# Optimization experiments

Measured on AMD Instinct MI355X. Metric: run time of the kernel, lower is better.

The kernel has to match this reference:

```python
import jax, jax.numpy as jnp
import numpy as np

EPS = 1e-12  # torch F.normalize clamp_min eps


def _linear_interp(t, M):
    # PyTorch F.interpolate(mode='linear', align_corners=False) along last axis.
    L = t.shape[-1]
    src = (jnp.arange(M, dtype=t.dtype) + 0.5) * (L / M) - 0.5
    src = jnp.maximum(src, 0.0)
    i0 = jnp.minimum(jnp.floor(src).astype(jnp.int32), L - 1)
    i1 = jnp.minimum(i0 + 1, L - 1)
    frac = src - i0.astype(t.dtype)
    return t[..., i0] * (1.0 - frac) + t[..., i1] * frac


def _l2norm(t):
    n = jnp.linalg.norm(t, axis=-1, keepdims=True)
    return t / jnp.maximum(n, EPS)


def setup_inputs() -> dict:
    key = jax.random.key(0)
    ks = jax.random.split(key, 6)
    b, dim, m = 4, 512, 4096
    h = w = 64
    heads = 8
    s = 0.02
    return {
        "x": jax.random.normal(ks[0], (b, dim, m), dtype=jnp.float32),
        "y": jax.random.normal(ks[1], (b, dim, h, w), dtype=jnp.float32),
        "temperature": jnp.ones((heads, 1, 1), dtype=jnp.float32),
        "w_kv": jax.random.normal(ks[2], (2 * dim, dim), dtype=jnp.float32) * s,
        "w_q": jax.random.normal(ks[3], (dim, dim), dtype=jnp.float32) * s,
        "w_dw": jax.random.normal(ks[4], (dim, dim, 3, 3), dtype=jnp.float32) * s,
        "w_out": jax.random.normal(ks[5], (dim, dim), dtype=jnp.float32) * s,
    }


def reference(x, y, temperature, w_kv, w_q, w_dw, w_out):
    b, c, m = x.shape
    heads = temperature.shape[0]
    hd = c // heads

    # kv = Conv1d(dim, 2*dim, k=1)(x); split into k, v
    kv = jnp.einsum('bcm,oc->bom', x, w_kv)
    k, v = jnp.split(kv, 2, axis=1)

    # q = dwconv3x3(Conv2d 1x1(y)) -> flatten -> linear-resize to m
    q = jnp.einsum('bchw,oc->bohw', y, w_q)
    q = jax.lax.conv_general_dilated(
        q, w_dw, window_strides=(1, 1), padding=[(1, 1), (1, 1)],
        dimension_numbers=('NCHW', 'OIHW', 'NCHW'))
    q = q.reshape(b, c, -1)
    q = _linear_interp(q, m)

    # split heads: [b, head, c', m]
    q = _l2norm(q.reshape(b, heads, hd, m))
    k = _l2norm(k.reshape(b, heads, hd, m))
    v = v.reshape(b, heads, hd, m)

    # channel-wise attention: [b, head, c', c']
    attn = jnp.einsum('bhcm,bhdm->bhcd', q, k) * temperature
    attn = jax.nn.softmax(attn, axis=-1)
    out = jnp.einsum('bhcd,bhdm->bhcm', attn, v).reshape(b, c, m)

    # project_out: Conv1d k=1
    return jnp.einsum('bcm,oc->bom', out, w_out)
```

## Files before the change

kernel.cpp:

```cpp
#include <hip/hip_runtime.h>
#include <hip/hip_bf16.h>
#include <math.h>

typedef float f32x4 __attribute__((ext_vector_type(4)));
typedef int   i32x4 __attribute__((ext_vector_type(4)));
typedef short s16x8 __attribute__((ext_vector_type(8)));

#define NB 4
#define NC 512
#define NM 4096
#define NHEADS 8

__device__ __forceinline__ float b2f(unsigned short u) {
  union { unsigned int i; float f; } x; x.i = ((unsigned)u) << 16; return x.f;
}

__global__ __launch_bounds__(256) void transpose_k(
    const float* __restrict__ x, const float* __restrict__ y,
    __hip_bfloat16* __restrict__ xT, __hip_bfloat16* __restrict__ yT)
{
  __shared__ __hip_bfloat16 tile[64][65];
  int z = blockIdx.z;
  const float* src = ((z < 4) ? x : y) + (long)(z & 3) * ((long)NC * NM);
  __hip_bfloat16* dst = (z < 4 ? xT : yT) + (long)(z & 3) * ((long)NC * NM);
  int tm = blockIdx.x * 64, tc = blockIdx.y * 64;
  int tx = threadIdx.x & 63, ty = threadIdx.x >> 6;
  #pragma unroll
  for (int p = 0; p < 16; p++) {
    int row = ty + p * 4;
    tile[row][tx] = __float2bfloat16(src[(long)(tc + row) * NM + tm + tx]);
  }
  __syncthreads();
  #pragma unroll
  for (int p = 0; p < 16; p++) {
    int row = ty + p * 4;
    dst[(long)(tm + row) * NC + tc + tx] = tile[tx][row];
  }
}

__global__ __launch_bounds__(256) void pack_wdw(
    const float* __restrict__ wdw, __hip_bfloat16* __restrict__ Wr)
{
  long idx = (long)blockIdx.x * 256 + threadIdx.x;
  if (idx < 9L * 512 * 512) {
    int r = (int)(idx >> 18);
    int rem = (int)(idx & 262143);
    int o = rem >> 9, i = rem & 511;
    Wr[idx] = __float2bfloat16(wdw[((long)o * 512 + i) * 9 + r]);
  }
}

__global__ __launch_bounds__(256) void convert_w(
    const float* __restrict__ wkv, const float* __restrict__ wq,
    __hip_bfloat16* __restrict__ wkvB, __hip_bfloat16* __restrict__ wqB)
{
  long idx = (long)blockIdx.x * 256 + threadIdx.x;
  if (idx < 524288) {
    wkvB[idx] = __float2bfloat16(wkv[idx]);
  } else if (idx < 524288 + 262144) {
    long j = idx - 524288;
    wqB[j] = __float2bfloat16(wq[j]);
  }
}

__global__ __launch_bounds__(256) void gemm_bt(
    const __hip_bfloat16* __restrict__ Aall, long sA,
    const __hip_bfloat16* __restrict__ Ball, long sB,
    __hip_bfloat16* __restrict__ Cball, float* __restrict__ Cfall, long sC,
    int M, int N, int Kd, int outF32)
{
  const __hip_bfloat16* A = Aall + (long)blockIdx.z * sA;
  const __hip_bfloat16* B = Ball + (long)blockIdx.z * sB;
  const int m0 = blockIdx.y * 128, n0 = blockIdx.x * 128;
  __shared__ __hip_bfloat16 As[128 * 40];
  __shared__ __hip_bfloat16 Bs[128 * 40];
  const int tid = threadIdx.x;
  const int wid = tid >> 6, lane = tid & 63;
  const int wm = (wid >> 1) * 64, wn = (wid & 1) * 64;
  const int quad = lane >> 4, l16 = lane & 15;
  const int srow = tid >> 2, scol = (tid & 3) * 8;
  f32x4 acc[4][4] = {};
  const __hip_bfloat16* pA0 = A + (long)(m0 + srow) * Kd + scol;
  const __hip_bfloat16* pA1 = pA0 + (long)64 * Kd;
  const __hip_bfloat16* pB0 = B + (long)(n0 + srow) * Kd + scol;
  const __hip_bfloat16* pB1 = pB0 + (long)64 * Kd;
  i32x4 va0 = *(const i32x4*)(pA0);
  i32x4 va1 = *(const i32x4*)(pA1);
  i32x4 vb0 = *(const i32x4*)(pB0);
  i32x4 vb1 = *(const i32x4*)(pB1);
  for (int k0 = 0; k0 < Kd; k0 += 32) {
    __syncthreads();
    *(i32x4*)(&As[srow * 40 + scol])        = va0;
    *(i32x4*)(&As[(srow + 64) * 40 + scol]) = va1;
    *(i32x4*)(&Bs[srow * 40 + scol])        = vb0;
    *(i32x4*)(&Bs[(srow + 64) * 40 + scol]) = vb1;
    if (k0 + 32 < Kd) {
      va0 = *(const i32x4*)(pA0 + k0 + 32);
      va1 = *(const i32x4*)(pA1 + k0 + 32);
      vb0 = *(const i32x4*)(pB0 + k0 + 32);
      vb1 = *(const i32x4*)(pB1 + k0 + 32);
    }
    __syncthreads();
    s16x8 bfr[4];
    #pragma unroll
    for (int j = 0; j < 4; j++)
      bfr[j] = *(const s16x8*)(&Bs[(wn + j * 16 + l16) * 40 + quad * 8]);
    #pragma unroll
    for (int i = 0; i < 4; i++) {
      s16x8 af = *(const s16x8*)(&As[(wm + i * 16 + l16) * 40 + quad * 8]);
      #pragma unroll
      for (int j = 0; j < 4; j++)
        acc[i][j] = __builtin_amdgcn_mfma_f32_16x16x32_bf16(af, bfr[j], acc[i][j], 0, 0, 0);
    }
  }
  if (outF32) {
    float* C = Cfall + (long)blockIdx.z * sC;
    #pragma unroll
    for (int i = 0; i < 4; i++)
      #pragma unroll
      for (int j = 0; j < 4; j++) {
        int rbase = m0 + wm + i * 16 + quad * 4;
        int col = n0 + wn + j * 16 + l16;
        #pragma unroll
        for (int r = 0; r < 4; r++)
          C[(long)(rbase + r) * N + col] = acc[i][j][r];
      }
  } else {
    __hip_bfloat16* C = Cball + (long)blockIdx.z * sC;
    #pragma unroll
    for (int i = 0; i < 4; i++)
      #pragma unroll
      for (int j = 0; j < 4; j++) {
        int rbase = m0 + wm + i * 16 + quad * 4;
        int col = n0 + wn + j * 16 + l16;
        #pragma unroll
        for (int r = 0; r < 4; r++)
          C[(long)(rbase + r) * N + col] = __float2bfloat16(acc[i][j][r]);
      }
  }
}

__global__ __launch_bounds__(256) void conv3x3(
    const __hip_bfloat16* __restrict__ Wr,
    const __hip_bfloat16* __restrict__ q1t,
    __hip_bfloat16* __restrict__ q2)
{
  const int b = blockIdx.z;
  const int n0 = blockIdx.x * 128;
  const int m0 = blockIdx.y * 128;
  __shared__ __hip_bfloat16 As[128 * 40];
  __shared__ __hip_bfloat16 Bs[256 * 40];
  const int tid = threadIdx.x;
  const int wid = tid >> 6, lane = tid & 63;
  const int wm = (wid >> 1) * 64, wn = (wid & 1) * 64;
  const int quad = lane >> 4, l16 = lane & 15;
  const int srow = tid >> 2, scol = (tid & 3) * 8;
  const int h0 = n0 >> 6;
  const __hip_bfloat16* qb = q1t + (long)b * NM * NC;
  f32x4 acc[4][4] = {};
  const s16x8 zero8 = {0, 0, 0, 0, 0, 0, 0, 0};

  for (int ic = 0; ic < 512; ic += 32) {
    __syncthreads();
    #pragma unroll
    for (int rr = 0; rr < 4; rr++) {
      int p = rr * 64 + srow;
      int hw = (h0 - 1) * 64 + p;
      i32x4 val = {};
      if (hw >= 0 && hw < NM) val = *(const i32x4*)(&qb[(long)hw * NC + ic + scol]);
      *(i32x4*)(&Bs[p * 40 + scol]) = val;
    }
    for (int r = 0; r < 9; r++) {
      int dy = r / 3 - 1, dx = r % 3 - 1;
      __syncthreads();
      *(i32x4*)(&As[srow * 40 + scol]) =
          *(const i32x4*)(&Wr[((long)r * 512 + m0 + srow) * 512 + ic + scol]);
      *(i32x4*)(&As[(srow + 64) * 40 + scol]) =
          *(const i32x4*)(&Wr[((long)r * 512 + m0 + srow + 64) * 512 + ic + scol]);
      __syncthreads();
      s16x8 bfr[4];
      #pragma unroll
      for (int j = 0; j < 4; j++) {
        int nl = wn + j * 16 + l16;
        int wq = nl & 63, hr = nl >> 6;
        int wp = wq + dx;
        bool v = ((unsigned)wp) < 64u;
        int p = v ? ((hr + 1 + dy) * 64 + wp) : 0;
        s16x8 t = *(const s16x8*)(&Bs[p * 40 + quad * 8]);
        bfr[j] = v ? t : zero8;
      }
      #pragma unroll
      for (int i = 0; i < 4; i++) {
        s16x8 af = *(const s16x8*)(&As[(wm + i * 16 + l16) * 40 + quad * 8]);
        #pragma unroll
        for (int j = 0; j < 4; j++)
          acc[i][j] = __builtin_amdgcn_mfma_f32_16x16x32_bf16(af, bfr[j], acc[i][j], 0, 0, 0);
      }
    }
  }
  __hip_bfloat16* Cb = q2 + (long)b * NC * NM;
  #pragma unroll
  for (int i = 0; i < 4; i++) {
    #pragma unroll
    for (int j = 0; j < 4; j++) {
      int rbase = m0 + wm + i * 16 + quad * 4;
      int col = n0 + wn + j * 16 + l16;
      #pragma unroll
      for (int r = 0; r < 4; r++)
        Cb[(long)(rbase + r) * NM + col] = __float2bfloat16(acc[i][j][r]);
    }
  }
}

__global__ __launch_bounds__(256) void rowsumsq(
    const __hip_bfloat16* __restrict__ X, float* __restrict__ out)
{
  long row = blockIdx.x;
  const __hip_bfloat16* p = X + row * (long)NM + threadIdx.x * 16;
  union { i32x4 v; unsigned short u[8]; } a, b;
  a.v = *(const i32x4*)(p);
  b.v = *(const i32x4*)(p + 8);
  float s = 0.f;
  #pragma unroll
  for (int t = 0; t < 8; t++) {
    float f0 = b2f(a.u[t]); s += f0 * f0;
    float f1 = b2f(b.u[t]); s += f1 * f1;
  }
  #pragma unroll
  for (int off = 32; off > 0; off >>= 1) s += __shfl_down(s, off);
  __shared__ float red[4];
  if ((threadIdx.x & 63) == 0) red[threadIdx.x >> 6] = s;
  __syncthreads();
  if (threadIdx.x == 0)
    out[row] = fmaxf(sqrtf(red[0] + red[1] + red[2] + red[3]), 1e-12f);
}

__global__ __launch_bounds__(256) void attn_g(
    const __hip_bfloat16* __restrict__ q2, const __hip_bfloat16* __restrict__ Kb,
    float* __restrict__ Gpart)
{
  const int mc = blockIdx.x, h = blockIdx.y, b = blockIdx.z;
  const __hip_bfloat16* qrow = q2 + ((long)b * NC + h * 64) * NM + mc * 512;
  const __hip_bfloat16* krow = Kb + ((long)b * NC + h * 64) * NM + mc * 512;
  __shared__ __hip_bfloat16 Qs[64 * 40];
  __shared__ __hip_bfloat16 Ks[64 * 40];
  const int tid = threadIdx.x;
  const int wid = tid >> 6, lane = tid & 63;
  const int wc = (wid >> 1) * 32, wd = (wid & 1) * 32;
  const int quad = lane >> 4, l16 = lane & 15;
  const int srow = tid >> 2, scol = (tid & 3) * 8;
  f32x4 acc[2][2] = {};
  for (int k0 = 0; k0 < 512; k0 += 32) {
    __syncthreads();
    *(i32x4*)(&Qs[srow * 40 + scol]) = *(const i32x4*)(&qrow[(long)srow * NM + k0 + scol]);
    *(i32x4*)(&Ks[srow * 40 + scol]) = *(const i32x4*)(&krow[(long)srow * NM + k0 + scol]);
    __syncthreads();
    s16x8 bfr[2];
    #pragma unroll
    for (int j = 0; j < 2; j++)
      bfr[j] = *(const s16x8*)(&Ks[(wd + j * 16 + l16) * 40 + quad * 8]);
    #pragma unroll
    for (int i = 0; i < 2; i++) {
      s16x8 af = *(const s16x8*)(&Qs[(wc + i * 16 + l16) * 40 + quad * 8]);
      #pragma unroll
      for (int j = 0; j < 2; j++)
        acc[i][j] = __builtin_amdgcn_mfma_f32_16x16x32_bf16(af, bfr[j], acc[i][j], 0, 0, 0);
    }
  }
  float* gp = Gpart + ((long)((b * 8 + h) * 8 + mc)) * 4096;
  #pragma unroll
  for (int i = 0; i < 2; i++)
    #pragma unroll
    for (int j = 0; j < 2; j++)
      #pragma unroll
      for (int r = 0; r < 4; r++)
        gp[(wc + i * 16 + quad * 4 + r) * 64 + wd + j * 16 + l16] = acc[i][j][r];
}

__global__ __launch_bounds__(256) void softmax_attn(
    const float* __restrict__ Gpart, const float* __restrict__ qn,
    const float* __restrict__ kn, const float* __restrict__ temp,
    float* __restrict__ attn)
{
  const int h = blockIdx.x, b = blockIdx.y;
  __shared__ float G[64][64];
  const int tid = threadIdx.x;
  const float tv = temp[h];
  for (int e = tid; e < 4096; e += 256) {
    float s = 0.f;
    #pragma unroll
    for (int p = 0; p < 8; p++)
      s += Gpart[((long)((b * 8 + h) * 8 + p)) * 4096 + e];
    int c = e >> 6, d = e & 63;
    float scale = tv / (qn[b * 512 + h * 64 + c] * kn[b * 512 + h * 64 + d]);
    G[c][d] = s * scale;
  }
  __syncthreads();
  int row = tid >> 2, s4 = tid & 3;
  float mx = -1e30f;
  for (int d = s4; d < 64; d += 4) mx = fmaxf(mx, G[row][d]);
  mx = fmaxf(mx, __shfl_xor(mx, 1));
  mx = fmaxf(mx, __shfl_xor(mx, 2));
  float sum = 0.f;
  for (int d = s4; d < 64; d += 4) { float e = __expf(G[row][d] - mx); G[row][d] = e; sum += e; }
  sum += __shfl_xor(sum, 1);
  sum += __shfl_xor(sum, 2);
  float inv = 1.f / sum;
  float* ap = attn + ((long)(b * 8 + h)) * 4096;
  for (int d = s4; d < 64; d += 4) ap[row * 64 + d] = G[row][d] * inv;
}

__global__ __launch_bounds__(256) void wa_kernel(
    const float* __restrict__ attn, const float* __restrict__ wout,
    __hip_bfloat16* __restrict__ Wa)
{
  const int oc = blockIdx.x, h = blockIdx.y, b = blockIdx.z;
  __shared__ float At[64][64];
  __shared__ float Wt[64][65];
  const int tid = threadIdx.x;
  const float* ap = attn + ((long)(b * 8 + h)) * 4096;
  for (int e = tid; e < 4096; e += 256) {
    At[e >> 6][e & 63] = ap[e];
    Wt[e >> 6][e & 63] = wout[(long)(oc * 64 + (e >> 6)) * 512 + h * 64 + (e & 63)];
  }
  __syncthreads();
  int d = tid & 63, og = tid >> 6;
  #pragma unroll
  for (int k = 0; k < 16; k++) {
    int o = og * 16 + k;
    float s = 0.f;
    #pragma unroll 8
    for (int c = 0; c < 64; c++) s += Wt[o][c] * At[c][d];
    Wa[((long)b * 512 + oc * 64 + o) * 512 + h * 64 + d] = __float2bfloat16(s);
  }
}

extern "C" void kernel_launch(void* const* d_in, const int* in_sizes, int n_in,
                              void* d_out, int out_size, void* d_ws, size_t ws_size,
                              hipStream_t stream) {
  const float* x    = (const float*)d_in[0];
  const float* y    = (const float*)d_in[1];
  const float* temp = (const float*)d_in[2];
  const float* wkv  = (const float*)d_in[3];
  const float* wq   = (const float*)d_in[4];
  const float* wdw  = (const float*)d_in[5];
  const float* wout = (const float*)d_in[6];
  float* out = (float*)d_out;

  char* ws = (char*)d_ws;
  const long TEN = 16777216;
  __hip_bfloat16* xT  = (__hip_bfloat16*)(ws);
  __hip_bfloat16* q2  = xT;
  __hip_bfloat16* yT  = (__hip_bfloat16*)(ws + TEN);
  float* Gpart        = (float*)(ws + TEN);
  float* attn         = (float*)(ws + TEN + 4194304);
  __hip_bfloat16* Wa  = (__hip_bfloat16*)(ws + TEN + 4718592);
  float* knorm        = (float*)(ws + TEN + 6815744);
  float* qnorm        = (float*)(ws + TEN + 6823936);
  __hip_bfloat16* Kb  = (__hip_bfloat16*)(ws + 2 * TEN);
  __hip_bfloat16* Vt  = (__hip_bfloat16*)(ws + 3 * TEN);
  __hip_bfloat16* q1t = (__hip_bfloat16*)(ws + 4 * TEN);
  __hip_bfloat16* Wr  = (__hip_bfloat16*)(ws + 5 * TEN);
  __hip_bfloat16* wkvB = (__hip_bfloat16*)(ws + 5 * TEN + 4718592);
  __hip_bfloat16* wqB  = (__hip_bfloat16*)(ws + 5 * TEN + 5767168);

  const long S = (long)4096 * 512;
  dim3 blk(256);

  pack_wdw<<<dim3(9216), blk, 0, stream>>>(wdw, Wr);
  convert_w<<<dim3(3072), blk, 0, stream>>>(wkv, wq, wkvB, wqB);
  transpose_k<<<dim3(64, 8, 8), blk, 0, stream>>>(x, y, xT, yT);
  gemm_bt<<<dim3(32, 4, 4), blk, 0, stream>>>(wkvB, 0L, xT, S, Kb, nullptr, S, 512, 4096, 512, 0);
  gemm_bt<<<dim3(4, 32, 4), blk, 0, stream>>>(xT, S, wkvB + 512 * 512, 0L, Vt, nullptr, S, 4096, 512, 512, 0);
  gemm_bt<<<dim3(4, 32, 4), blk, 0, stream>>>(yT, S, wqB, 0L, q1t, nullptr, S, 4096, 512, 512, 0);
  conv3x3<<<dim3(32, 4, 4), blk, 0, stream>>>(Wr, q1t, q2);
  rowsumsq<<<dim3(2048), blk, 0, stream>>>(Kb, knorm);
  rowsumsq<<<dim3(2048), blk, 0, stream>>>(q2, qnorm);
  attn_g<<<dim3(8, 8, 4), blk, 0, stream>>>(q2, Kb, Gpart);
  softmax_attn<<<dim3(8, 4), blk, 0, stream>>>(Gpart, qnorm, knorm, temp, attn);
  wa_kernel<<<dim3(8, 8, 4), blk, 0, stream>>>(attn, wout, Wa);
  gemm_bt<<<dim3(32, 4, 4), blk, 0, stream>>>(Wa, (long)512 * 512, Vt, S, nullptr, out, S, 512, 4096, 512, 1);
  (void)in_sizes; (void)n_in; (void)out_size; (void)ws_size;
}
```

Baseline: 341.6 us.

## Fold 1x1 q projection into 3x3 conv weights and use direct global-to-LDS loads

Precomputes folded weights Wfold[r] = Wdw[r] @ Wq with a small batched GEMM, so the conv reads yT directly and the per-batch q1 projection GEMM is dropped. GEMM and conv tile loads now use global_load_lds straight into unpadded LDS, replacing register-staged copies. The conv also stages three taps of weights per barrier to cut synchronisation. In exchange, the software prefetch overlap is lost (loads wait before compute), the unpadded LDS layout may cause bank conflicts, and folding changes bf16 rounding.

After: 321.5 us. 1.06x faster.

```diff
diff --git a/kernel.cpp b/kernel.cpp
--- a/kernel.cpp
+++ b/kernel.cpp
@@ -10,6 +10,10 @@
 #define NC 512
 #define NM 4096
 #define NHEADS 8
+
+#define GLDS16(src, dst) __builtin_amdgcn_global_load_lds( \
+    (const __attribute__((address_space(1))) void*)(src),  \
+    (__attribute__((address_space(3))) void*)(dst), 16, 0, 0)
 
 __device__ __forceinline__ float b2f(unsigned short u) {
   union { unsigned int i; float f; } x; x.i = ((unsigned)u) << 16; return x.f;
@@ -52,14 +56,15 @@
 
 __global__ __launch_bounds__(256) void convert_w(
     const float* __restrict__ wkv, const float* __restrict__ wq,
-    __hip_bfloat16* __restrict__ wkvB, __hip_bfloat16* __restrict__ wqB)
+    __hip_bfloat16* __restrict__ wkvB, __hip_bfloat16* __restrict__ wqT)
 {
   long idx = (long)blockIdx.x * 256 + threadIdx.x;
   if (idx < 524288) {
     wkvB[idx] = __float2bfloat16(wkv[idx]);
   } else if (idx < 524288 + 262144) {
     long j = idx - 524288;
-    wqB[j] = __float2bfloat16(wq[j]);
+    int c = (int)(j >> 9), cp = (int)(j & 511);
+    wqT[j] = __float2bfloat16(wq[(long)cp * 512 + c]);
   }
 }
 
@@ -72,42 +77,33 @@
   const __hip_bfloat16* A = Aall + (long)blockIdx.z * sA;
   const __hip_bfloat16* B = Ball + (long)blockIdx.z * sB;
   const int m0 = blockIdx.y * 128, n0 = blockIdx.x * 128;
-  __shared__ __hip_bfloat16 As[128 * 40];
-  __shared__ __hip_bfloat16 Bs[128 * 40];
+  __shared__ __hip_bfloat16 As[128 * 32];
+  __shared__ __hip_bfloat16 Bs[128 * 32];
   const int tid = threadIdx.x;
   const int wid = tid >> 6, lane = tid & 63;
   const int wm = (wid >> 1) * 64, wn = (wid & 1) * 64;
   const int quad = lane >> 4, l16 = lane & 15;
-  const int srow = tid >> 2, scol = (tid & 3) * 8;
+  const int srow = wid * 32 + (lane >> 2);
+  const int scol = (lane & 3) * 8;
   f32x4 acc[4][4] = {};
-  const __hip_bfloat16* pA0 = A + (long)(m0 + srow) * Kd + scol;
-  const __hip_bfloat16* pA1 = pA0 + (long)64 * Kd;
-  const __hip_bfloat16* pB0 = B + (long)(n0 + srow) * Kd + scol;
-  const __hip_bfloat16* pB1 = pB0 + (long)64 * Kd;
-  i32x4 va0 = *(const i32x4*)(pA0);
-  i32x4 va1 = *(const i32x4*)(pA1);
-  i32x4 vb0 = *(const i32x4*)(pB0);
-  i32x4 vb1 = *(const i32x4*)(pB1);
   for (int k0 = 0; k0 < Kd; k0 += 32) {
     __syncthreads();
-    *(i32x4*)(&As[srow * 40 + scol])        = va0;
-    *(i32x4*)(&As[(srow + 64) * 40 + scol]) = va1;
-    *(i32x4*)(&Bs[srow * 40 + scol])        = vb0;
-    *(i32x4*)(&Bs[(srow + 64) * 40 + scol]) = vb1;
-    if (k0 + 32 < Kd) {
-      va0 = *(const i32x4*)(pA0 + k0 + 32);
-      va1 = *(const i32x4*)(pA1 + k0 + 32);
-      vb0 = *(const i32x4*)(pB0 + k0 + 32);
-      vb1 = *(const i32x4*)(pB1 + k0 + 32);
-    }
+    #pragma unroll
+    for (int t = 0; t < 2; t++) {
+      GLDS16(A + (long)(m0 + srow + t * 16) * Kd + k0 + scol,
+             As + (wid * 32 + t * 16) * 32);
+      GLDS16(B + (long)(n0 + srow + t * 16) * Kd + k0 + scol,
+             Bs + (wid * 32 + t * 16) * 32);
+    }
+    __builtin_amdgcn_s_waitcnt(0);
     __syncthreads();
     s16x8 bfr[4];
     #pragma unroll
     for (int j = 0; j < 4; j++)
-      bfr[j] = *(const s16x8*)(&Bs[(wn + j * 16 + l16) * 40 + quad * 8]);
+      bfr[j] = *(const s16x8*)(&Bs[(wn + j * 16 + l16) * 32 + quad * 8]);
     #pragma unroll
     for (int i = 0; i < 4; i++) {
-      s16x8 af = *(const s16x8*)(&As[(wm + i * 16 + l16) * 40 + quad * 8]);
+      s16x8 af = *(const s16x8*)(&As[(wm + i * 16 + l16) * 32 + quad * 8]);
       #pragma unroll
       for (int j = 0; j < 4; j++)
         acc[i][j] = __builtin_amdgcn_mfma_f32_16x16x32_bf16(af, bfr[j], acc[i][j], 0, 0, 0);
@@ -141,60 +137,73 @@
 }
 
 __global__ __launch_bounds__(256) void conv3x3(
-    const __hip_bfloat16* __restrict__ Wr,
-    const __hip_bfloat16* __restrict__ q1t,
+    const __hip_bfloat16* __restrict__ Wt,
+    const __hip_bfloat16* __restrict__ yT,
+    const __hip_bfloat16* __restrict__ zeropad,
     __hip_bfloat16* __restrict__ q2)
 {
   const int b = blockIdx.z;
   const int n0 = blockIdx.x * 128;
   const int m0 = blockIdx.y * 128;
-  __shared__ __hip_bfloat16 As[128 * 40];
-  __shared__ __hip_bfloat16 Bs[256 * 40];
+  __shared__ __hip_bfloat16 As3[3 * 128 * 32];
+  __shared__ __hip_bfloat16 Bs[256 * 32];
   const int tid = threadIdx.x;
   const int wid = tid >> 6, lane = tid & 63;
   const int wm = (wid >> 1) * 64, wn = (wid & 1) * 64;
   const int quad = lane >> 4, l16 = lane & 15;
-  const int srow = tid >> 2, scol = (tid & 3) * 8;
+  const int lrow = lane >> 2, scol = (lane & 3) * 8;
   const int h0 = n0 >> 6;
-  const __hip_bfloat16* qb = q1t + (long)b * NM * NC;
+  const __hip_bfloat16* yb = yT + (long)b * NM * NC;
   f32x4 acc[4][4] = {};
   const s16x8 zero8 = {0, 0, 0, 0, 0, 0, 0, 0};
 
   for (int ic = 0; ic < 512; ic += 32) {
-    __syncthreads();
-    #pragma unroll
-    for (int rr = 0; rr < 4; rr++) {
-      int p = rr * 64 + srow;
-      int hw = (h0 - 1) * 64 + p;
-      i32x4 val = {};
-      if (hw >= 0 && hw < NM) val = *(const i32x4*)(&qb[(long)hw * NC + ic + scol]);
-      *(i32x4*)(&Bs[p * 40 + scol]) = val;
-    }
-    for (int r = 0; r < 9; r++) {
-      int dy = r / 3 - 1, dx = r % 3 - 1;
+    #pragma unroll
+    for (int g = 0; g < 3; g++) {
       __syncthreads();
-      *(i32x4*)(&As[srow * 40 + scol]) =
-          *(const i32x4*)(&Wr[((long)r * 512 + m0 + srow) * 512 + ic + scol]);
-      *(i32x4*)(&As[(srow + 64) * 40 + scol]) =
-          *(const i32x4*)(&Wr[((long)r * 512 + m0 + srow + 64) * 512 + ic + scol]);
+      if (g == 0) {
+        #pragma unroll
+        for (int t = 0; t < 4; t++) {
+          int p = wid * 64 + t * 16 + lrow;
+          int hw = (h0 - 1) * 64 + p;
+          const __hip_bfloat16* src = (((unsigned)hw) < (unsigned)NM)
+              ? (yb + (long)hw * NC + ic + scol) : (zeropad + scol % 8);
+          GLDS16(src, Bs + (wid * 64 + t * 16) * 32);
+        }
+      }
+      #pragma unroll
+      for (int t = 0; t < 3; t++) {
+        int r = g * 3 + t;
+        #pragma unroll
+        for (int t2 = 0; t2 < 2; t2++) {
+          GLDS16(Wt + ((long)r * 512 + m0 + wid * 32 + t2 * 16 + lrow) * 512 + ic + scol,
+                 As3 + (t * 128 + wid * 32 + t2 * 16) * 32);
+        }
+      }
+      __builtin_amdgcn_s_waitcnt(0);
       __syncthreads();
-      s16x8 bfr[4];
-      #pragma unroll
-      for (int j = 0; j < 4; j++) {
-        int nl = wn + j * 16 + l16;
-        int wq = nl & 63, hr = nl >> 6;
-        int wp = wq + dx;
-        bool v = ((unsigned)wp) < 64u;
-        int p = v ? ((hr + 1 + dy) * 64 + wp) : 0;
-        s16x8 t = *(const s16x8*)(&Bs[p * 40 + quad * 8]);
-        bfr[j] = v ? t : zero8;
-      }
-      #pragma unroll
-      for (int i = 0; i < 4; i++) {
-        s16x8 af = *(const s16x8*)(&As[(wm + i * 16 + l16) * 40 + quad * 8]);
-        #pragma unroll
-        for (int j = 0; j < 4; j++)
-          acc[i][j] = __builtin_amdgcn_mfma_f32_16x16x32_bf16(af, bfr[j], acc[i][j], 0, 0, 0);
+      const int dy = g - 1;
+      #pragma unroll
+      for (int t = 0; t < 3; t++) {
+        const int dx = t - 1;
+        s16x8 bfr[4];
+        #pragma unroll
+        for (int j = 0; j < 4; j++) {
+          int nl = wn + j * 16 + l16;
+          int wq_ = nl & 63, hr = nl >> 6;
+          int wp = wq_ + dx;
+          bool v = ((unsigned)wp) < 64u;
+          int p = v ? ((hr + 1 + dy) * 64 + wp) : 0;
+          s16x8 tt = *(const s16x8*)(&Bs[p * 32 + quad * 8]);
+          bfr[j] = v ? tt : zero8;
+        }
+        #pragma unroll
+        for (int i = 0; i < 4; i++) {
+          s16x8 af = *(const s16x8*)(&As3[(t * 128 + wm + i * 16 + l16) * 32 + quad * 8]);
+          #pragma unroll
+          for (int j = 0; j < 4; j++)
+            acc[i][j] = __builtin_amdgcn_mfma_f32_16x16x32_bf16(af, bfr[j], acc[i][j], 0, 0, 0);
+        }
       }
     }
   }
@@ -316,12 +325,12 @@
 {
   const int oc = blockIdx.x, h = blockIdx.y, b = blockIdx.z;
   __shared__ float At[64][64];
-  __shared__ float Wt[64][65];
+  __shared__ float Wtl[64][65];
   const int tid = threadIdx.x;
   const float* ap = attn + ((long)(b * 8 + h)) * 4096;
   for (int e = tid; e < 4096; e += 256) {
     At[e >> 6][e & 63] = ap[e];
-    Wt[e >> 6][e & 63] = wout[(long)(oc * 64 + (e >> 6)) * 512 + h * 64 + (e & 63)];
+    Wtl[e >> 6][e & 63] = wout[(long)(oc * 64 + (e >> 6)) * 512 + h * 64 + (e & 63)];
   }
   __syncthreads();
   int d = tid & 63, og = tid >> 6;
@@ -330,7 +339,7 @@
     int o = og * 16 + k;
     float s = 0.f;
     #pragma unroll 8
-    for (int c = 0; c < 64; c++) s += Wt[o][c] * At[c][d];
+    for (int c = 0; c < 64; c++) s += Wtl[o][c] * At[c][d];
     Wa[((long)b * 512 + oc * 64 + o) * 512 + h * 64 + d] = __float2bfloat16(s);
   }
 }
@@ -359,26 +368,29 @@
   float* qnorm        = (float*)(ws + TEN + 6823936);
   __hip_bfloat16* Kb  = (__hip_bfloat16*)(ws + 2 * TEN);
   __hip_bfloat16* Vt  = (__hip_bfloat16*)(ws + 3 * TEN);
-  __hip_bfloat16* q1t = (__hip_bfloat16*)(ws + 4 * TEN);
-  __hip_bfloat16* Wr  = (__hip_bfloat16*)(ws + 5 * TEN);
-  __hip_bfloat16* wkvB = (__hip_bfloat16*)(ws + 5 * TEN + 4718592);
-  __hip_bfloat16* wqB  = (__hip_bfloat16*)(ws + 5 * TEN + 5767168);
+  __hip_bfloat16* Wfold = (__hip_bfloat16*)(ws + 4 * TEN);
+  __hip_bfloat16* Wr    = (__hip_bfloat16*)(ws + 4 * TEN + 4718592);
+  __hip_bfloat16* wkvB  = (__hip_bfloat16*)(ws + 4 * TEN + 9437184);
+  __hip_bfloat16* wqT   = (__hip_bfloat16*)(ws + 4 * TEN + 10485760);
+  __hip_bfloat16* zeropad = (__hip_bfloat16*)(ws + 4 * TEN + 11010048);
 
   const long S = (long)4096 * 512;
+  const long S2 = (long)512 * 512;
   dim3 blk(256);
 
+  hipMemsetAsync(zeropad, 0, 256, stream);
   pack_wdw<<<dim3(9216), blk, 0, stream>>>(wdw, Wr);
-  convert_w<<<dim3(3072), blk, 0, stream>>>(wkv, wq, wkvB, wqB);
+  convert_w<<<dim3(3072), blk, 0, stream>>>(wkv, wq, wkvB, wqT);
   transpose_k<<<dim3(64, 8, 8), blk, 0, stream>>>(x, y, xT, yT);
+  gemm_bt<<<dim3(4, 4, 9), blk, 0, stream>>>(Wr, S2, wqT, 0L, Wfold, nullptr, S2, 512, 512, 512, 0);
   gemm_bt<<<dim3(32, 4, 4), blk, 0, stream>>>(wkvB, 0L, xT, S, Kb, nullptr, S, 512, 4096, 512, 0);
   gemm_bt<<<dim3(4, 32, 4), blk, 0, stream>>>(xT, S, wkvB + 512 * 512, 0L, Vt, nullptr, S, 4096, 512, 512, 0);
-  gemm_bt<<<dim3(4, 32, 4), blk, 0, stream>>>(yT, S, wqB, 0L, q1t, nullptr, S, 4096, 512, 512, 0);
-  conv3x3<<<dim3(32, 4, 4), blk, 0, stream>>>(Wr, q1t, q2);
+  conv3x3<<<dim3(32, 4, 4), blk, 0, stream>>>(Wfold, yT, zeropad, q2);
   rowsumsq<<<dim3(2048), blk, 0, stream>>>(Kb, knorm);
   rowsumsq<<<dim3(2048), blk, 0, stream>>>(q2, qnorm);
   attn_g<<<dim3(8, 8, 4), blk, 0, stream>>>(q2, Kb, Gpart);
   softmax_attn<<<dim3(8, 4), blk, 0, stream>>>(Gpart, qnorm, knorm, temp, attn);
   wa_kernel<<<dim3(8, 8, 4), blk, 0, stream>>>(attn, wout, Wa);
-  gemm_bt<<<dim3(32, 4, 4), blk, 0, stream>>>(Wa, (long)512 * 512, Vt, S, nullptr, out, S, 512, 4096, 512, 1);
+  gemm_bt<<<dim3(32, 4, 4), blk, 0, stream>>>(Wa, S2, Vt, S, nullptr, out, S, 512, 4096, 512, 1);
   (void)in_sizes; (void)n_in; (void)out_size; (void)ws_size;
 }
```
